# Kernel optimization log

Measured on AMD Instinct MI355X. Metric: run time of the kernel, lower is better.

## Reference

```python
import jax, jax.numpy as jnp
import numpy as np

B, N, M = 64, 256, 16
H_A = 256
DMIN, DMAX, STEP = 0.0, 3.0, 0.2
N_FILTERS = 16  # arange(0, 3.0+0.2, 0.2) -> 16 gaussians, == h_b
N_CONV = 3
N_CLASSES = 6
IN_DIM = 2 * H_A + N_FILTERS  # 528
EPS = 1e-5


def _bn(x, gamma, beta):
    # BatchNorm1d in training mode: batch stats over all but last axis, biased var
    axes = tuple(range(x.ndim - 1))
    mu = jnp.mean(x, axis=axes, keepdims=True)
    var = jnp.var(x, axis=axes, keepdims=True)
    return (x - mu) * jax.lax.rsqrt(var + EPS) * gamma + beta


def setup_inputs() -> dict:
    key = jax.random.key(0)
    ks = jax.random.split(key, 10)
    nbr_adj_dist = jax.random.uniform(ks[0], (B, N, M), dtype=jnp.float32) * DMAX
    nbr_adj_list = jax.random.randint(ks[1], (B, N, M), 0, N, dtype=jnp.int32)
    emb_table = jax.random.normal(ks[2], (N, H_A), dtype=jnp.float32)
    s = 1.0 / np.sqrt(IN_DIM)
    W_full = jax.random.uniform(ks[3], (N_CONV, IN_DIM, 2 * H_A), minval=-s, maxval=s, dtype=jnp.float32)
    b_full = jax.random.uniform(ks[4], (N_CONV, 2 * H_A), minval=-s, maxval=s, dtype=jnp.float32)
    g_h = jnp.ones((N_CONV, 2 * H_A), jnp.float32)
    beta_h = jnp.zeros((N_CONV, 2 * H_A), jnp.float32)
    g_o = jnp.ones((N_CONV, H_A), jnp.float32)
    beta_o = jnp.zeros((N_CONV, H_A), jnp.float32)
    sc = 1.0 / np.sqrt(H_A)
    W_cls = jax.random.uniform(ks[5], (H_A, N_CLASSES), minval=-sc, maxval=sc, dtype=jnp.float32)
    b_cls = jax.random.uniform(ks[6], (N_CLASSES,), minval=-sc, maxval=sc, dtype=jnp.float32)
    return {"nbr_adj_dist": nbr_adj_dist, "nbr_adj_list": nbr_adj_list,
            "emb_table": emb_table, "W_full": W_full, "b_full": b_full,
            "g_h": g_h, "beta_h": beta_h, "g_o": g_o, "beta_o": beta_o,
            "W_cls": W_cls, "b_cls": b_cls}


def reference(nbr_adj_dist, nbr_adj_list, emb_table, W_full, b_full,
              g_h, beta_h, g_o, beta_o, W_cls, b_cls):
    # Gaussian distance expansion -> bond embedding [B,N,M,h_b]
    filters = jnp.arange(DMIN, DMAX + STEP, STEP, dtype=jnp.float32)
    nbr_emb = jnp.exp(-((nbr_adj_dist[..., None] - filters) ** 2) / (STEP ** 2))

    # atom embedding of arange(N), broadcast over batch -> [B,N,h_a]
    atom_emb = jnp.broadcast_to(emb_table[None], (B, N, H_A))

    idx = nbr_adj_list.reshape(B, N * M, 1)
    for l in range(N_CONV):
        # gather neighbor atom embeddings [B,N,M,h_a]
        atom_nbr = jnp.take_along_axis(atom_emb, idx, axis=1).reshape(B, N, M, H_A)
        self_emb = jnp.broadcast_to(atom_emb[:, :, None, :], (B, N, M, H_A))
        total = jnp.concatenate([self_emb, atom_nbr, nbr_emb], axis=-1)  # [B,N,M,528]
        z = jnp.einsum('bnmi,io->bnmo', total, W_full[l]) + b_full[l]
        z = _bn(z, g_h[l], beta_h[l])
        nbr_filter, nbr_core = jnp.split(z, 2, axis=-1)
        nbr_sumed = jnp.sum(jax.nn.sigmoid(nbr_filter) * jax.nn.relu(nbr_core), axis=2)
        nbr_sumed = _bn(nbr_sumed, g_o[l], beta_o[l])
        atom_emb = jax.nn.relu(atom_emb + nbr_sumed)

    atom_emb = jax.nn.relu(atom_emb)
    pooled = jnp.sum(atom_emb, axis=1) / N  # pooling by num_atoms
    logits = pooled @ W_cls + b_cls
    return jax.nn.softmax(logits, axis=-1)
```

## Files before the change

kernel.cpp:

```cpp
#include <hip/hip_runtime.h>
#include <math.h>

#define NB 64
#define NA 256
#define NM 16
#define HA 256
#define NF 16
#define NCONV 3
#define NCLS 6
#define EPSB 1e-5f

typedef __attribute__((ext_vector_type(8))) short short8v;
typedef __attribute__((ext_vector_type(4))) float f32x4;

__device__ __forceinline__ short f2bf(float x) {
  union { float f; unsigned u; } v; v.f = x;
  unsigned r = v.u + 0x7fff + ((v.u >> 16) & 1);
  return (short)(r >> 16);
}

__global__ void prep_weights(const float* __restrict__ Wf,
                             short* __restrict__ WT, short* __restrict__ W3bf) {
  int i = blockIdx.x * 256 + threadIdx.x;
  const int TOT1 = NCONV * 1024 * 256;
  if (i < TOT1) {
    int l = i / (1024 * 256);
    int r = i - l * (1024 * 256);
    int o = r >> 8, k = r & 255;
    float w = (o < 512) ? Wf[(l * 528 + k) * 512 + o]
                        : Wf[(l * 528 + 256 + k) * 512 + (o - 512)];
    WT[i] = f2bf(w);
  }
  const int TOT2 = NCONV * 512 * NF;
  if (i < TOT2) {
    int l = i / (512 * NF);
    int r = i - l * (512 * NF);
    int o = r >> 4, k = r & 15;
    W3bf[i] = f2bf(Wf[(l * 528 + 512 + k) * 512 + o]);
  }
}

__global__ void gauss_kernel(const float* __restrict__ dist, short* __restrict__ Gbf) {
  int i = blockIdx.x * 256 + threadIdx.x;
  int r = i >> 4, f = i & 15;
  float d = dist[r];
  float x = d - 0.2f * (float)f;
  Gbf[i] = f2bf(__expf(-x * x * 25.0f));
}

__global__ void init_atom(const float* __restrict__ emb, float* __restrict__ atom) {
  int i = blockIdx.x * 256 + threadIdx.x;
  atom[i] = emb[i & (NA * HA - 1)];
}

__global__ void emb_bf(const float* __restrict__ emb, short* __restrict__ ebf) {
  int i = blockIdx.x * 256 + threadIdx.x;
  ebf[i] = f2bf(emb[i]);
}

__global__ __launch_bounds__(256) void gemm_mfma(const short* __restrict__ Abf,
                                                 const short* __restrict__ WT,
                                                 float* __restrict__ C, int Mrows) {
  __shared__ short As[128][72];
  __shared__ short Bs[128][72];
  int t = threadIdx.x;
  int wave = t >> 6, lane = t & 63;
  int wr = wave >> 1, wc = wave & 1;
  int l16 = lane & 15, lhi = lane >> 4;

  int wg = blockIdx.x;
  int nRowBlocks = Mrows >> 7;
  int rowBlock, colBlock;
  if (nRowBlocks >= 8) {
    rowBlock = (wg & 7) + ((wg >> 6) << 3);
    colBlock = (wg >> 3) & 7;
  } else {
    rowBlock = wg % nRowBlocks;
    colBlock = wg / nRowBlocks;
  }
  int rowBase = rowBlock << 7, colBase = colBlock << 7;

  f32x4 acc[4][4];
#pragma unroll
  for (int i = 0; i < 4; ++i)
#pragma unroll
    for (int j = 0; j < 4; ++j) acc[i][j] = (f32x4)(0.f);

  for (int k0 = 0; k0 < 256; k0 += 64) {
#pragma unroll
    for (int cc = 0; cc < 4; ++cc) {
      int c = t + cc * 256;
      int row = c >> 3, ko = (c & 7) << 3;
      *(int4*)&As[row][ko] = *(const int4*)&Abf[(size_t)(rowBase + row) * 256 + k0 + ko];
      *(int4*)&Bs[row][ko] = *(const int4*)&WT[(size_t)(colBase + row) * 256 + k0 + ko];
    }
    __syncthreads();
#pragma unroll
    for (int ks = 0; ks < 2; ++ks) {
      int kk = ks * 32 + lhi * 8;
      short8v a[4], b[4];
#pragma unroll
      for (int f = 0; f < 4; ++f) {
        a[f] = *(const short8v*)&As[wr * 64 + f * 16 + l16][kk];
        b[f] = *(const short8v*)&Bs[wc * 64 + f * 16 + l16][kk];
      }
#pragma unroll
      for (int i = 0; i < 4; ++i)
#pragma unroll
        for (int j = 0; j < 4; ++j)
          acc[i][j] = __builtin_amdgcn_mfma_f32_16x16x32_bf16(a[i], b[j], acc[i][j], 0, 0, 0);
    }
    __syncthreads();
  }
#pragma unroll
  for (int i = 0; i < 4; ++i) {
#pragma unroll
    for (int j = 0; j < 4; ++j) {
      int col = colBase + wc * 64 + j * 16 + l16;
      int row0 = rowBase + wr * 64 + i * 16 + lhi * 4;
#pragma unroll
      for (int r = 0; r < 4; ++r)
        C[(size_t)(row0 + r) * 1024 + col] = acc[i][j][r];
    }
  }
}

__device__ __forceinline__ void decode_wg(int wg, int& b, int& n0) {
  int x = wg & 7;
  int t2 = wg >> 3;
  int ng = t2 & 31;
  int bhi = t2 >> 5;
  b = bhi * 8 + x;
  n0 = ng * 8;
}

template <int PASS>
__global__ __launch_bounds__(256, 3) void pass_mfma(const float* __restrict__ H,
                                                    const short* __restrict__ Gbf,
                                                    const int* __restrict__ adj,
                                                    const short* __restrict__ W3bf,
                                                    const float* __restrict__ coef,
                                                    float* __restrict__ nbr,
                                                    float* __restrict__ stats,
                                                    int batched) {
  __shared__ int jis[128];
  __shared__ float cf[1024];

  int t = threadIdx.x;
  int b, n0;
  decode_wg(blockIdx.x, b, n0);
  int hbase = batched ? b * NA : 0;

  if (t < 128) jis[t] = adj[(b * NA + n0) * NM + t];
  if (PASS == 1) {
    cf[t] = coef[t]; cf[256 + t] = coef[256 + t];
    cf[512 + t] = coef[512 + t]; cf[768 + t] = coef[768 + t];
  }
  __syncthreads();

  int lane = t & 63, wv = t >> 6;
  int l16 = lane & 15, lhi = lane >> 4;
  const short8v zv = {0, 0, 0, 0, 0, 0, 0, 0};

  short8v bfm[8];
  int oc[8];
#pragma unroll
  for (int j = 0; j < 8; ++j) {
    int col = wv * 64 + (j & 3) * 16 + l16 + ((j >= 4) ? 256 : 0);
    oc[j] = col;
    bfm[j] = (lhi < 2) ? *(const short8v*)&W3bf[(size_t)col * NF + lhi * 8] : zv;
  }

  float scf[4], shf[4], scc[4], shc[4];
  if (PASS == 1) {
#pragma unroll
    for (int p = 0; p < 4; ++p) {
      scf[p] = cf[oc[p]];       shf[p] = cf[512 + oc[p]];
      scc[p] = cf[oc[p + 4]];   shc[p] = cf[512 + oc[p + 4]];
    }
  }

  float s1f[4] = {0, 0, 0, 0}, s2f[4] = {0, 0, 0, 0};
  float s1c[4] = {0, 0, 0, 0}, s2c[4] = {0, 0, 0, 0};
  float sB1[4] = {0, 0, 0, 0}, sB2[4] = {0, 0, 0, 0};

  for (int nn = 0; nn < 8; ++nn) {
    int n = n0 + nn;
    short8v af = (lhi < 2)
        ? *(const short8v*)&Gbf[(((size_t)(b * NA + n)) * NM + l16) * NF + lhi * 8]
        : zv;
    f32x4 acc[8];
#pragma unroll
    for (int j = 0; j < 8; ++j) acc[j] = (f32x4)(0.f);
#pragma unroll
    for (int j = 0; j < 8; ++j)
      acc[j] = __builtin_amdgcn_mfma_f32_16x16x32_bf16(af, bfm[j], acc[j], 0, 0, 0);

    int jv[4];
#pragma unroll
    for (int r = 0; r < 4; ++r) jv[r] = jis[nn * 16 + lhi * 4 + r];
    const float* hs = &H[(size_t)(hbase + n) * 1024];
    float x1v[8];
#pragma unroll
    for (int j = 0; j < 8; ++j) x1v[j] = hs[oc[j]];
    float yv[8][4];
#pragma unroll
    for (int j = 0; j < 8; ++j)
#pragma unroll
      for (int r = 0; r < 4; ++r)
        yv[j][r] = H[(size_t)(hbase + jv[r]) * 1024 + 512 + oc[j]];

    if (PASS == 0) {
#pragma unroll
      for (int p = 0; p < 4; ++p) {
#pragma unroll
        for (int r = 0; r < 4; ++r) {
          float zf = acc[p][r] + x1v[p] + yv[p][r];
          float zc = acc[p + 4][r] + x1v[p + 4] + yv[p + 4][r];
          s1f[p] += zf; s2f[p] = fmaf(zf, zf, s2f[p]);
          s1c[p] += zc; s2c[p] = fmaf(zc, zc, s2c[p]);
        }
      }
    } else {
#pragma unroll
      for (int p = 0; p < 4; ++p) {
        float ps = 0.f;
#pragma unroll
        for (int r = 0; r < 4; ++r) {
          float zf = acc[p][r] + x1v[p] + yv[p][r];
          float zc = acc[p + 4][r] + x1v[p + 4] + yv[p + 4][r];
          float yfv = fmaf(zf, scf[p], shf[p]);
          float ycv = fmaf(zc, scc[p], shc[p]);
          float sig = 1.0f / (1.0f + __expf(-yfv));
          ps = fmaf(sig, fmaxf(ycv, 0.f), ps);
        }
        ps += __shfl_xor(ps, 16);
        ps += __shfl_xor(ps, 32);
        if (lhi == 0) {
          nbr[(size_t)(b * NA + n) * HA + oc[p]] = ps;
          sB1[p] += ps; sB2[p] = fmaf(ps, ps, sB2[p]);
        }
      }
    }
  }

  if (PASS == 0) {
#pragma unroll
    for (int p = 0; p < 4; ++p) {
      float v;
      v = s1f[p]; v += __shfl_xor(v, 16); v += __shfl_xor(v, 32);
      if (lhi == 0) atomicAdd(&stats[oc[p]], v);
      v = s2f[p]; v += __shfl_xor(v, 16); v += __shfl_xor(v, 32);
      if (lhi == 0) atomicAdd(&stats[512 + oc[p]], v);
      v = s1c[p]; v += __shfl_xor(v, 16); v += __shfl_xor(v, 32);
      if (lhi == 0) atomicAdd(&stats[oc[p + 4]], v);
      v = s2c[p]; v += __shfl_xor(v, 16); v += __shfl_xor(v, 32);
      if (lhi == 0) atomicAdd(&stats[512 + oc[p + 4]], v);
    }
  } else {
#pragma unroll
    for (int p = 0; p < 4; ++p) {
      if (lhi == 0) {
        atomicAdd(&stats[oc[p]], sB1[p]);
        atomicAdd(&stats[256 + oc[p]], sB2[p]);
      }
    }
  }
}

__global__ void finalize1(const float* __restrict__ bn1, const float* __restrict__ g,
                          const float* __restrict__ beta, float* __restrict__ coef) {
  int t = threadIdx.x;
  const float inv = 1.0f / (float)(NB * NA * NM);
  float mu = bn1[t] * inv;
  float var = bn1[512 + t] * inv - mu * mu;
  float sc = g[t] * rsqrtf(var + EPSB);
  coef[t] = sc;
  coef[512 + t] = beta[t] - mu * sc;
}

__global__ void finalize2(const float* __restrict__ bn2, const float* __restrict__ g,
                          const float* __restrict__ beta, float* __restrict__ coef2) {
  int t = threadIdx.x;
  const float inv = 1.0f / (float)(NB * NA);
  float mu = bn2[t] * inv;
  float var = bn2[256 + t] * inv - mu * mu;
  float sc = g[t] * rsqrtf(var + EPSB);
  coef2[t] = sc;
  coef2[256 + t] = beta[t] - mu * sc;
}

__global__ void pass_c(float4* __restrict__ atom, const float4* __restrict__ nbr,
                       const float* __restrict__ coef2, short* __restrict__ abf) {
  int i = blockIdx.x * 256 + threadIdx.x;
  int o = (i & 63) * 4;
  float4 a = atom[i];
  float4 nv = nbr[i];
  a.x = fmaxf(a.x + fmaf(nv.x, coef2[o + 0], coef2[256 + o + 0]), 0.f);
  a.y = fmaxf(a.y + fmaf(nv.y, coef2[o + 1], coef2[256 + o + 1]), 0.f);
  a.z = fmaxf(a.z + fmaf(nv.z, coef2[o + 2], coef2[256 + o + 2]), 0.f);
  a.w = fmaxf(a.w + fmaf(nv.w, coef2[o + 3], coef2[256 + o + 3]), 0.f);
  atom[i] = a;
  short4 s;
  s.x = f2bf(a.x); s.y = f2bf(a.y); s.z = f2bf(a.z); s.w = f2bf(a.w);
  *(short4*)&abf[(size_t)i * 4] = s;
}

__global__ __launch_bounds__(256) void epilogue(const float* __restrict__ atom,
                                                const float* __restrict__ Wc,
                                                const float* __restrict__ bc,
                                                float* __restrict__ out) {
  __shared__ float pooled[HA];
  __shared__ float lg[NCLS];
  int b = blockIdx.x, t = threadIdx.x;
  float s = 0.f;
  for (int n = 0; n < NA; ++n) s += atom[(size_t)(b * NA + n) * HA + t];
  pooled[t] = s * (1.0f / (float)NA);
  __syncthreads();
  if (t < NCLS) {
    float a = bc[t];
    for (int o = 0; o < HA; ++o) a += pooled[o] * Wc[o * NCLS + t];
    lg[t] = a;
  }
  __syncthreads();
  if (t == 0) {
    float mx = lg[0];
    for (int c = 1; c < NCLS; ++c) mx = fmaxf(mx, lg[c]);
    float e[NCLS], den = 0.f;
    for (int c = 0; c < NCLS; ++c) { e[c] = __expf(lg[c] - mx); den += e[c]; }
    for (int c = 0; c < NCLS; ++c) out[b * NCLS + c] = e[c] / den;
  }
}

extern "C" void kernel_launch(void* const* d_in, const int* in_sizes, int n_in,
                              void* d_out, int out_size, void* d_ws, size_t ws_size,
                              hipStream_t stream) {
  const float* dist = (const float*)d_in[0];
  const int* adj = (const int*)d_in[1];
  const float* emb = (const float*)d_in[2];
  const float* Wf = (const float*)d_in[3];
  const float* gh = (const float*)d_in[5];
  const float* bh = (const float*)d_in[6];
  const float* go = (const float*)d_in[7];
  const float* bo = (const float*)d_in[8];
  const float* Wc = (const float*)d_in[9];
  const float* bc = (const float*)d_in[10];
  float* out = (float*)d_out;

  char* p = (char*)d_ws;
  short* Gbf = (short*)p;   p += (size_t)NB * NA * NM * NF * 2;
  float* H = (float*)p;     p += (size_t)NB * NA * 1024 * 4;
  float* H0 = (float*)p;    p += (size_t)NA * 1024 * 4;
  float* atom = (float*)p;  p += (size_t)NB * NA * HA * 4;
  float* nbr = (float*)p;   p += (size_t)NB * NA * HA * 4;
  short* WT = (short*)p;    p += (size_t)NCONV * 1024 * 256 * 2;
  short* Abf = (short*)p;   p += (size_t)NB * NA * 256 * 2;
  short* Ebf = (short*)p;   p += (size_t)NA * 256 * 2;
  short* W3bf = (short*)p;  p += (size_t)NCONV * 512 * NF * 2;
  float* bn1 = (float*)p;   p += 1024 * 4;
  float* bn2 = (float*)p;   p += 512 * 4;
  float* coef1 = (float*)p; p += 1024 * 4;
  float* coef2 = (float*)p; p += 512 * 4;

  prep_weights<<<3072, 256, 0, stream>>>(Wf, WT, W3bf);
  gauss_kernel<<<16384, 256, 0, stream>>>(dist, Gbf);
  init_atom<<<16384, 256, 0, stream>>>(emb, atom);
  emb_bf<<<256, 256, 0, stream>>>(emb, Ebf);

  for (int l = 0; l < NCONV; ++l) {
    hipMemsetAsync(bn1, 0, (1024 + 512) * 4, stream);
    int Mrows = (l == 0) ? NA : NB * NA;
    const short* Amat = (l == 0) ? Ebf : Abf;
    float* Hl = (l == 0) ? H0 : H;
    gemm_mfma<<<(Mrows / 128) * 8, 256, 0, stream>>>(Amat, WT + (size_t)l * 1024 * 256, Hl, Mrows);
    pass_mfma<0><<<2048, 256, 0, stream>>>(Hl, Gbf, adj, W3bf + (size_t)l * 512 * NF,
                                           nullptr, nullptr, bn1, l > 0);
    finalize1<<<1, 512, 0, stream>>>(bn1, gh + l * 512, bh + l * 512, coef1);
    pass_mfma<1><<<2048, 256, 0, stream>>>(Hl, Gbf, adj, W3bf + (size_t)l * 512 * NF,
                                           coef1, nbr, bn2, l > 0);
    finalize2<<<1, 256, 0, stream>>>(bn2, go + l * 256, bo + l * 256, coef2);
    pass_c<<<4096, 256, 0, stream>>>((float4*)atom, (const float4*)nbr, coef2, Abf);
  }
  epilogue<<<NB, 256, 0, stream>>>(atom, Wc, bc, out);
}
```

Baseline: 546.4 us.

## Vectorize column mapping in pass kernels and replicate BN stat accumulators

Lanes are remapped so each one owns four consecutive output columns instead of strided ones. This lets the H gathers, the coefficient loads and the nbr stores use float4 accesses, and it removes the shared-memory coefficient staging. BatchNorm statistic atomics are spread over 8 replicated buffers, picked by block index, to reduce contention, and the finalize kernels sum the replicas. In exchange the memset grows and finalize reads more data.

```diff
diff --git a/kernel.cpp b/kernel.cpp
--- a/kernel.cpp
+++ b/kernel.cpp
@@ -9,6 +9,7 @@
 #define NCONV 3
 #define NCLS 6
 #define EPSB 1e-5f
+#define NREP 8
 
 typedef __attribute__((ext_vector_type(8))) short short8v;
 typedef __attribute__((ext_vector_type(4))) float f32x4;
@@ -144,45 +145,35 @@
                                                     float* __restrict__ stats,
                                                     int batched) {
   __shared__ int jis[128];
-  __shared__ float cf[1024];
-
   int t = threadIdx.x;
   int b, n0;
   decode_wg(blockIdx.x, b, n0);
   int hbase = batched ? b * NA : 0;
-
   if (t < 128) jis[t] = adj[(b * NA + n0) * NM + t];
-  if (PASS == 1) {
-    cf[t] = coef[t]; cf[256 + t] = coef[256 + t];
-    cf[512 + t] = coef[512 + t]; cf[768 + t] = coef[768 + t];
-  }
   __syncthreads();
 
   int lane = t & 63, wv = t >> 6;
   int l16 = lane & 15, lhi = lane >> 4;
   const short8v zv = {0, 0, 0, 0, 0, 0, 0, 0};
+  int ocb = wv * 64 + l16 * 4;
 
   short8v bfm[8];
-  int oc[8];
 #pragma unroll
   for (int j = 0; j < 8; ++j) {
-    int col = wv * 64 + (j & 3) * 16 + l16 + ((j >= 4) ? 256 : 0);
-    oc[j] = col;
+    int col = ocb + (j & 3) + ((j >= 4) ? 256 : 0);
     bfm[j] = (lhi < 2) ? *(const short8v*)&W3bf[(size_t)col * NF + lhi * 8] : zv;
   }
 
-  float scf[4], shf[4], scc[4], shc[4];
+  f32x4 scf, shf, scc, shc;
   if (PASS == 1) {
-#pragma unroll
-    for (int p = 0; p < 4; ++p) {
-      scf[p] = cf[oc[p]];       shf[p] = cf[512 + oc[p]];
-      scc[p] = cf[oc[p + 4]];   shc[p] = cf[512 + oc[p + 4]];
-    }
-  }
-
-  float s1f[4] = {0, 0, 0, 0}, s2f[4] = {0, 0, 0, 0};
-  float s1c[4] = {0, 0, 0, 0}, s2c[4] = {0, 0, 0, 0};
-  float sB1[4] = {0, 0, 0, 0}, sB2[4] = {0, 0, 0, 0};
+    scf = *(const f32x4*)&coef[ocb];        shf = *(const f32x4*)&coef[512 + ocb];
+    scc = *(const f32x4*)&coef[256 + ocb];  shc = *(const f32x4*)&coef[768 + ocb];
+  }
+
+  float* st = stats + (blockIdx.x & (NREP - 1)) * (PASS == 0 ? 1024 : 512);
+
+  f32x4 s1f = (f32x4)(0.f), s2f = (f32x4)(0.f), s1c = (f32x4)(0.f), s2c = (f32x4)(0.f);
+  f32x4 sB1 = (f32x4)(0.f), sB2 = (f32x4)(0.f);
 
   for (int nn = 0; nn < 8; ++nn) {
     int n = n0 + nn;
@@ -200,35 +191,36 @@
 #pragma unroll
     for (int r = 0; r < 4; ++r) jv[r] = jis[nn * 16 + lhi * 4 + r];
     const float* hs = &H[(size_t)(hbase + n) * 1024];
-    float x1v[8];
-#pragma unroll
-    for (int j = 0; j < 8; ++j) x1v[j] = hs[oc[j]];
-    float yv[8][4];
-#pragma unroll
-    for (int j = 0; j < 8; ++j)
-#pragma unroll
-      for (int r = 0; r < 4; ++r)
-        yv[j][r] = H[(size_t)(hbase + jv[r]) * 1024 + 512 + oc[j]];
+    f32x4 x1f = *(const f32x4*)&hs[ocb];
+    f32x4 x1c = *(const f32x4*)&hs[ocb + 256];
+    f32x4 yf[4], yc[4];
+#pragma unroll
+    for (int r = 0; r < 4; ++r) {
+      const float* hr = &H[(size_t)(hbase + jv[r]) * 1024 + 512];
+      yf[r] = *(const f32x4*)&hr[ocb];
+      yc[r] = *(const f32x4*)&hr[ocb + 256];
+    }
 
     if (PASS == 0) {
 #pragma unroll
       for (int p = 0; p < 4; ++p) {
 #pragma unroll
         for (int r = 0; r < 4; ++r) {
-          float zf = acc[p][r] + x1v[p] + yv[p][r];
-          float zc = acc[p + 4][r] + x1v[p + 4] + yv[p + 4][r];
+          float zf = acc[p][r] + x1f[p] + yf[r][p];
+          float zc = acc[p + 4][r] + x1c[p] + yc[r][p];
           s1f[p] += zf; s2f[p] = fmaf(zf, zf, s2f[p]);
           s1c[p] += zc; s2c[p] = fmaf(zc, zc, s2c[p]);
         }
       }
     } else {
+      f32x4 pp;
 #pragma unroll
       for (int p = 0; p < 4; ++p) {
         float ps = 0.f;
 #pragma unroll
         for (int r = 0; r < 4; ++r) {
-          float zf = acc[p][r] + x1v[p] + yv[p][r];
-          float zc = acc[p + 4][r] + x1v[p + 4] + yv[p + 4][r];
+          float zf = acc[p][r] + x1f[p] + yf[r][p];
+          float zc = acc[p + 4][r] + x1c[p] + yc[r][p];
           float yfv = fmaf(zf, scf[p], shf[p]);
           float ycv = fmaf(zc, scc[p], shc[p]);
           float sig = 1.0f / (1.0f + __expf(-yfv));
@@ -236,10 +228,12 @@
         }
         ps += __shfl_xor(ps, 16);
         ps += __shfl_xor(ps, 32);
-        if (lhi == 0) {
-          nbr[(size_t)(b * NA + n) * HA + oc[p]] = ps;
-          sB1[p] += ps; sB2[p] = fmaf(ps, ps, sB2[p]);
-        }
+        pp[p] = ps;
+      }
+      if (lhi == 0) {
+        *(f32x4*)&nbr[(size_t)(b * NA + n) * HA + ocb] = pp;
+        sB1 += pp;
+        sB2 += pp * pp;
       }
     }
   }
@@ -249,20 +243,20 @@
     for (int p = 0; p < 4; ++p) {
       float v;
       v = s1f[p]; v += __shfl_xor(v, 16); v += __shfl_xor(v, 32);
-      if (lhi == 0) atomicAdd(&stats[oc[p]], v);
+      if (lhi == 0) atomicAdd(&st[ocb + p], v);
       v = s2f[p]; v += __shfl_xor(v, 16); v += __shfl_xor(v, 32);
-      if (lhi == 0) atomicAdd(&stats[512 + oc[p]], v);
+      if (lhi == 0) atomicAdd(&st[512 + ocb + p], v);
       v = s1c[p]; v += __shfl_xor(v, 16); v += __shfl_xor(v, 32);
-      if (lhi == 0) atomicAdd(&stats[oc[p + 4]], v);
+      if (lhi == 0) atomicAdd(&st[256 + ocb + p], v);
       v = s2c[p]; v += __shfl_xor(v, 16); v += __shfl_xor(v, 32);
-      if (lhi == 0) atomicAdd(&stats[512 + oc[p + 4]], v);
+      if (lhi == 0) atomicAdd(&st[768 + ocb + p], v);
     }
   } else {
-#pragma unroll
-    for (int p = 0; p < 4; ++p) {
-      if (lhi == 0) {
-        atomicAdd(&stats[oc[p]], sB1[p]);
-        atomicAdd(&stats[256 + oc[p]], sB2[p]);
+    if (lhi == 0) {
+#pragma unroll
+      for (int p = 0; p < 4; ++p) {
+        atomicAdd(&st[ocb + p], sB1[p]);
+        atomicAdd(&st[256 + ocb + p], sB2[p]);
       }
     }
   }
@@ -271,9 +265,15 @@
 __global__ void finalize1(const float* __restrict__ bn1, const float* __restrict__ g,
                           const float* __restrict__ beta, float* __restrict__ coef) {
   int t = threadIdx.x;
+  float s1 = 0.f, s2 = 0.f;
+#pragma unroll
+  for (int r = 0; r < NREP; ++r) {
+    s1 += bn1[r * 1024 + t];
+    s2 += bn1[r * 1024 + 512 + t];
+  }
   const float inv = 1.0f / (float)(NB * NA * NM);
-  float mu = bn1[t] * inv;
-  float var = bn1[512 + t] * inv - mu * mu;
+  float mu = s1 * inv;
+  float var = s2 * inv - mu * mu;
   float sc = g[t] * rsqrtf(var + EPSB);
   coef[t] = sc;
   coef[512 + t] = beta[t] - mu * sc;
@@ -282,9 +282,15 @@
 __global__ void finalize2(const float* __restrict__ bn2, const float* __restrict__ g,
                           const float* __restrict__ beta, float* __restrict__ coef2) {
   int t = threadIdx.x;
+  float s1 = 0.f, s2 = 0.f;
+#pragma unroll
+  for (int r = 0; r < NREP; ++r) {
+    s1 += bn2[r * 512 + t];
+    s2 += bn2[r * 512 + 256 + t];
+  }
   const float inv = 1.0f / (float)(NB * NA);
-  float mu = bn2[t] * inv;
-  float var = bn2[256 + t] * inv - mu * mu;
+  float mu = s1 * inv;
+  float var = s2 * inv - mu * mu;
   float sc = g[t] * rsqrtf(var + EPSB);
   coef2[t] = sc;
   coef2[256 + t] = beta[t] - mu * sc;
@@ -357,8 +363,8 @@
   short* Abf = (short*)p;   p += (size_t)NB * NA * 256 * 2;
   short* Ebf = (short*)p;   p += (size_t)NA * 256 * 2;
   short* W3bf = (short*)p;  p += (size_t)NCONV * 512 * NF * 2;
-  float* bn1 = (float*)p;   p += 1024 * 4;
-  float* bn2 = (float*)p;   p += 512 * 4;
+  float* bn1 = (float*)p;   p += (size_t)NREP * 1024 * 4;
+  float* bn2 = (float*)p;   p += (size_t)NREP * 512 * 4;
   float* coef1 = (float*)p; p += 1024 * 4;
   float* coef2 = (float*)p; p += 512 * 4;
 
@@ -368,7 +374,7 @@
   emb_bf<<<256, 256, 0, stream>>>(emb, Ebf);
 
   for (int l = 0; l < NCONV; ++l) {
-    hipMemsetAsync(bn1, 0, (1024 + 512) * 4, stream);
+    hipMemsetAsync(bn1, 0, (size_t)NREP * (1024 + 512) * 4, stream);
     int Mrows = (l == 0) ? NA : NB * NA;
     const short* Amat = (l == 0) ? Ebf : Abf;
     float* Hl = (l == 0) ? H0 : H;
```

New measurement: 1.955 ms. 258% more time.
